# Kernel tuning notes

Hardware: AMD Instinct MI355X
Metric: run time of the kernel (lower is better)

Reference implementation:

```python
import jax, jax.numpy as jnp
import numpy as np

DIM = 1024
HEADS = 16
B, N = 4, 2048


def setup_inputs() -> dict:
    key = jax.random.key(0)
    ks = jax.random.split(key, 6)
    scale = DIM ** -0.5
    return {
        "x": jax.random.normal(ks[0], (B, N, DIM), dtype=jnp.float32),
        "mask": jax.random.randint(ks[1], (B, N, N), 0, 2) > 0,
        "Wqkv": jax.random.normal(ks[2], (DIM, 3 * DIM), dtype=jnp.float32) * scale,
        "bqkv": jax.random.normal(ks[3], (3 * DIM,), dtype=jnp.float32) * 0.02,
        "Wproj": jax.random.normal(ks[4], (DIM, DIM), dtype=jnp.float32) * scale,
        "bproj": jax.random.normal(ks[5], (DIM,), dtype=jnp.float32) * 0.02,
    }


def reference(x, mask, Wqkv, bqkv, Wproj, bproj):
    Bs, Ns, C = x.shape
    H = HEADS
    D = C // H
    scale = D ** -0.5
    qkv = x @ Wqkv + bqkv                       # [B, N, 3C]
    qkv = qkv.reshape(Bs, Ns, 3, H, D)          # split (three h d)
    q, k, v = jnp.moveaxis(qkv, 2, 0)           # each [B, N, H, D]
    q = q.transpose(0, 2, 1, 3)                 # [B, H, N, D]
    k = k.transpose(0, 2, 1, 3)
    v = v.transpose(0, 2, 1, 3)
    attn = jnp.einsum("bhnd,bhmd->bhnm", q, k) * scale  # [B, H, N, N]
    attn = jnp.where(mask[:, None, :, :], -jnp.inf, attn)
    attn = jax.nn.softmax(attn, axis=-1)
    out = jnp.einsum("bhnm,bhmd->bhnd", attn, v)        # [B, H, N, D]
    out = out.transpose(0, 2, 1, 3).reshape(Bs, Ns, C)  # [B, N, C]
    return out @ Wproj + bproj
```

## Files before the change

### kernel.cpp

```cpp
#include <hip/hip_runtime.h>
#include <cstdint>
#include <cstddef>

constexpr int kC = 1024;
constexpr int kH = 16;
constexpr int kB = 4;
constexpr int kN = 2048;
constexpr int kD = 64;

typedef unsigned short u16;
typedef unsigned int   u32;
typedef unsigned long long u64;
typedef __bf16 v8bf  __attribute__((ext_vector_type(8)));
typedef float  v4f   __attribute__((ext_vector_type(4)));
typedef u16    u16x8 __attribute__((ext_vector_type(8)));
typedef u16    u16x4 __attribute__((ext_vector_type(4)));

__device__ inline u16 f2bf(float f) {
    union { float f; unsigned u; } v; v.f = f;
    unsigned r = v.u + 0x7FFFu + ((v.u >> 16) & 1u);
    return (u16)(r >> 16);
}

__device__ inline void gl2lds16(const u16* g, u16* l) {
    __builtin_amdgcn_global_load_lds(
        (const __attribute__((address_space(1))) void*)g,
        (__attribute__((address_space(3))) void*)l, 16, 0, 0);
}

__global__ __launch_bounds__(256) void cast_bf16_kernel(
    const float* __restrict__ in, u16* __restrict__ outp)
{
    const int i = blockIdx.x * 256 + threadIdx.x;
    const float4 f = ((const float4*)in)[i];
    u16x4 o;
    o.x = f2bf(f.x); o.y = f2bf(f.y); o.z = f2bf(f.z); o.w = f2bf(f.w);
    ((u16x4*)outp)[i] = o;
}

__global__ __launch_bounds__(256) void tpose_cast_kernel(
    const float* __restrict__ W, u16* __restrict__ Wt, int R, int Cc)
{
    __shared__ u16 tile[64][65];
    const int c0 = blockIdx.x * 64;
    const int r0 = blockIdx.y * 64;
    const int t  = threadIdx.x;
#pragma unroll
    for (int it = 0; it < 16; ++it) {
        const int r = it * 4 + (t >> 6);
        const int c = t & 63;
        tile[c][r] = f2bf(W[(size_t)(r0 + r) * Cc + c0 + c]);
    }
    __syncthreads();
#pragma unroll
    for (int it = 0; it < 16; ++it) {
        const int rr = it * 4 + (t >> 6);
        const int cc = t & 63;
        Wt[(size_t)(c0 + rr) * R + r0 + cc] = tile[rr][cc];
    }
}

__global__ __launch_bounds__(256) void maskpack_kernel(
    const int* __restrict__ mask, u32* __restrict__ bits)
{
    const int seg  = blockIdx.x * 4 + (threadIdx.x >> 6);
    const int lane = threadIdx.x & 63;
    const size_t row = (size_t)(seg >> 5);
    const int s = seg & 31;
    const int m = mask[row * kN + s * 64 + lane];
    const u64 bal = __ballot(m != 0);
    if (lane == 0) ((u64*)bits)[row * 32 + s] = bal;
}

template <int MODE>
__global__ __launch_bounds__(256) void gemm_mfma_kernel(
    const u16* __restrict__ A, const u16* __restrict__ Bt,
    const float* __restrict__ bias, float* __restrict__ Cout,
    u16* __restrict__ qOut, u16* __restrict__ kOut, u16* __restrict__ vOut,
    int M, int N, int K)
{
    __shared__ u16 As[128 * 32];
    __shared__ u16 Bs[128 * 32];
    const int t    = threadIdx.x;
    const int w    = t >> 6;
    const int lane = t & 63;
    const int quad = lane >> 4;
    const int l16  = lane & 15;
    const int m0   = blockIdx.y * 128;
    const int n0   = blockIdx.x * 128;

    const int sr = lane >> 2;
    const int sk = (lane & 3) * 8;
    const u16* Ag0 = A  + (size_t)(m0 + 32 * w      + sr) * K + sk;
    const u16* Ag1 = A  + (size_t)(m0 + 32 * w + 16 + sr) * K + sk;
    const u16* Bg0 = Bt + (size_t)(n0 + 32 * w      + sr) * K + sk;
    const u16* Bg1 = Bt + (size_t)(n0 + 32 * w + 16 + sr) * K + sk;
    u16* Al0 = &As[(32 * w)      * 32];
    u16* Al1 = &As[(32 * w + 16) * 32];
    u16* Bl0 = &Bs[(32 * w)      * 32];
    u16* Bl1 = &Bs[(32 * w + 16) * 32];

    v4f acc[4][4];
#pragma unroll
    for (int r = 0; r < 4; ++r)
#pragma unroll
        for (int c = 0; c < 4; ++c) acc[r][c] = (v4f){0.f, 0.f, 0.f, 0.f};

    const int mrow = (w >> 1) * 64;
    const int ncol = (w & 1) * 64;

    for (int k0 = 0; k0 < K; k0 += 32) {
        __syncthreads();
        gl2lds16(Ag0 + k0, Al0);
        gl2lds16(Ag1 + k0, Al1);
        gl2lds16(Bg0 + k0, Bl0);
        gl2lds16(Bg1 + k0, Bl1);
        __syncthreads();

        v8bf af[4], bfr[4];
#pragma unroll
        for (int r = 0; r < 4; ++r)
            af[r] = *(const v8bf*)(&As[(mrow + r * 16 + l16) * 32 + quad * 8]);
#pragma unroll
        for (int c = 0; c < 4; ++c)
            bfr[c] = *(const v8bf*)(&Bs[(ncol + c * 16 + l16) * 32 + quad * 8]);
#pragma unroll
        for (int r = 0; r < 4; ++r)
#pragma unroll
            for (int c = 0; c < 4; ++c)
                acc[r][c] = __builtin_amdgcn_mfma_f32_16x16x32_bf16(
                    af[r], bfr[c], acc[r][c], 0, 0, 0);
    }

#pragma unroll
    for (int r = 0; r < 4; ++r) {
#pragma unroll
        for (int c = 0; c < 4; ++c) {
            const int col = n0 + ncol + c * 16 + l16;
            const float bv = bias[col];
#pragma unroll
            for (int reg = 0; reg < 4; ++reg) {
                const int row = m0 + mrow + r * 16 + quad * 4 + reg;
                const float val = acc[r][c][reg] + bv;
                if (MODE == 0) {
                    Cout[(size_t)row * N + col] = val;
                } else {
                    const int which = col >> 10;
                    const int rem   = col & 1023;
                    const int h     = rem >> 6;
                    const int d     = rem & 63;
                    const int b     = row >> 11;
                    const int n     = row & 2047;
                    u16* dst = (which == 0) ? qOut : (which == 1) ? kOut : vOut;
                    dst[(((size_t)(b * kH + h)) * kN + n) * kD + d] = f2bf(val);
                }
            }
        }
    }
}

__global__ __launch_bounds__(256, 3) void attn_mfma_kernel(
    const u16* __restrict__ q, const u16* __restrict__ k,
    const u16* __restrict__ v, const u32* __restrict__ mbits,
    u16* __restrict__ out)
{
    __shared__ u16 Ks[128 * 64];
    __shared__ u16 Vt[64 * 128];
    __shared__ u16 Ps[64 * 128];

    const int t    = threadIdx.x;
    const int w    = t >> 6;
    const int lane = t & 63;
    const int quad = lane >> 4;
    const int l16  = lane & 15;

    const int bh    = blockIdx.x >> 5;
    const int tile0 = (blockIdx.x & 31) * 64;
    const int b     = bh >> 4;
    const int h     = bh & 15;

    const u16* qb = q + (size_t)bh * kN * kD;
    const u16* kb = k + (size_t)bh * kN * kD;
    const u16* vb = v + (size_t)bh * kN * kD;

    const int qrow = tile0 + w * 16 + l16;
    const v8bf qf0 = *(const v8bf*)(qb + (size_t)qrow * kD + quad * 8);
    const v8bf qf1 = *(const v8bf*)(qb + (size_t)qrow * kD + 32 + quad * 8);

    const u32* mrowb = mbits + ((size_t)b * kN + qrow) * 64;

    const int skr  = t >> 1;
    const int skh  = t & 1;
    const int svk  = t >> 3;
    const int svd  = t & 7;
    const u16* kgp = kb + (size_t)skr * kD + skh * 32;
    const u16* vgp = vb + (size_t)(svk * 4) * kD + svd * 8;

    u16x8 kpre[4], vpre[4];
    uint4 mpre;
    auto prefetch = [&](int k0) {
        const u16x8* ks = (const u16x8*)(kgp + (size_t)k0 * kD);
        kpre[0] = ks[0]; kpre[1] = ks[1]; kpre[2] = ks[2]; kpre[3] = ks[3];
        const u16* vs = vgp + (size_t)k0 * kD;
        vpre[0] = *(const u16x8*)(vs);
        vpre[1] = *(const u16x8*)(vs + kD);
        vpre[2] = *(const u16x8*)(vs + 2 * kD);
        vpre[3] = *(const u16x8*)(vs + 3 * kD);
        mpre = *(const uint4*)(mrowb + (k0 >> 5));
    };

    v4f oacc[4];
#pragma unroll
    for (int i = 0; i < 4; ++i) oacc[i] = (v4f){0.f, 0.f, 0.f, 0.f};
    float rs = 0.f;

    prefetch(0);

    for (int kt = 0; kt < kN / 128; ++kt) {
        u16x8 kcur[4], vcur[4];
#pragma unroll
        for (int i = 0; i < 4; ++i) { kcur[i] = kpre[i]; vcur[i] = vpre[i]; }
        const uint4 mcur = mpre;
        const u32 mw[4] = {mcur.x, mcur.y, mcur.z, mcur.w};
        if (kt + 1 < kN / 128) prefetch((kt + 1) * 128);

        __syncthreads();

        {
            const int cb = skh * 4;
            u16* drow = &Ks[skr * 64];
#pragma unroll
            for (int i = 0; i < 4; ++i)
                *(u16x8*)(&drow[((cb + i) ^ (skr & 7)) * 8]) = kcur[i];
        }
        {
            const int blk = svk >> 1;
            const int off = (svk & 1) * 4;
#pragma unroll
            for (int j = 0; j < 8; ++j) {
                const int d = svd * 8 + j;
                u16x4 p;
                p.x = vcur[0][j]; p.y = vcur[1][j]; p.z = vcur[2][j]; p.w = vcur[3][j];
                *(u16x4*)(&Vt[d * 128 + ((blk ^ (d & 15)) * 8) + off]) = p;
            }
        }
        __syncthreads();

#pragma unroll
        for (int nb = 0; nb < 8; ++nb) {
            const int krow = nb * 16 + l16;
            const v8bf kf0 = *(const v8bf*)(&Ks[krow * 64 + ((quad       ^ (krow & 7)) * 8)]);
            const v8bf kf1 = *(const v8bf*)(&Ks[krow * 64 + (((quad + 4) ^ (krow & 7)) * 8)]);
            v4f s = (v4f){0.f, 0.f, 0.f, 0.f};
            s = __builtin_amdgcn_mfma_f32_16x16x32_bf16(kf0, qf0, s, 0, 0, 0);
            s = __builtin_amdgcn_mfma_f32_16x16x32_bf16(kf1, qf1, s, 0, 0, 0);

            const u32 m4 = (mw[nb >> 1] >> ((nb & 1) * 16 + quad * 4)) & 0xFu;
            const float e0 = (m4 & 1u) ? 0.f : __expf(s[0] * 0.125f);
            const float e1 = (m4 & 2u) ? 0.f : __expf(s[1] * 0.125f);
            const float e2 = (m4 & 4u) ? 0.f : __expf(s[2] * 0.125f);
            const float e3 = (m4 & 8u) ? 0.f : __expf(s[3] * 0.125f);
            rs += (e0 + e1) + (e2 + e3);

            u16x4 pw; pw.x = f2bf(e0); pw.y = f2bf(e1); pw.z = f2bf(e2); pw.w = f2bf(e3);
            const int pblk = nb * 2 + (quad >> 1);
            *(u16x4*)(&Ps[(w * 16 + l16) * 128 + ((pblk ^ l16) * 8) + (quad & 1) * 4]) = pw;
        }

#pragma unroll
        for (int ks = 0; ks < 4; ++ks) {
            const v8bf pa = *(const v8bf*)(&Ps[(w * 16 + l16) * 128 + (((ks * 4 + quad) ^ l16) * 8)]);
#pragma unroll
            for (int db = 0; db < 4; ++db) {
                const int d = db * 16 + l16;
                const v8bf vf = *(const v8bf*)(&Vt[d * 128 + (((ks * 4 + quad) ^ (d & 15)) * 8)]);
                oacc[db] = __builtin_amdgcn_mfma_f32_16x16x32_bf16(pa, vf, oacc[db], 0, 0, 0);
            }
        }
    }

    rs += __shfl_xor(rs, 16);
    rs += __shfl_xor(rs, 32);
    const float inv = 1.f / rs;
    float rq[4];
#pragma unroll
    for (int reg = 0; reg < 4; ++reg)
        rq[reg] = __shfl(inv, quad * 4 + reg);

#pragma unroll
    for (int db = 0; db < 4; ++db) {
#pragma unroll
        for (int reg = 0; reg < 4; ++reg) {
            const int row = tile0 + w * 16 + quad * 4 + reg;
            const int col = h * 64 + db * 16 + l16;
            out[((size_t)(b * kN + row)) * kC + col] = f2bf(oacc[db][reg] * rq[reg]);
        }
    }
}

extern "C" void kernel_launch(void* const* d_in, const int* in_sizes, int n_in,
                              void* d_out, int out_size, void* d_ws, size_t ws_size,
                              hipStream_t stream)
{
    const float* x     = (const float*)d_in[0];
    const int*   mask  = (const int*)d_in[1];
    const float* Wqkv  = (const float*)d_in[2];
    const float* bqkv  = (const float*)d_in[3];
    const float* Wproj = (const float*)d_in[4];
    const float* bproj = (const float*)d_in[5];
    float* out = (float*)d_out;

    const size_t nx = (size_t)kB * kN * kC;
    const size_t qkv_elems = (size_t)kB * kH * kN * kD;
    u16* xb     = (u16*)d_ws;
    u16* qbuf   = xb + nx;
    u16* kbuf   = qbuf + qkv_elems;
    u16* vbuf   = kbuf + qkv_elems;
    u16* aob    = vbuf + qkv_elems;
    u16* Wqkvt  = aob + nx;
    u16* Wprojt = Wqkvt + (size_t)3 * kC * kC;
    u32* mbits  = (u32*)(Wprojt + (size_t)kC * kC);

    maskpack_kernel<<<dim3(kB * kN * 32 / 4), dim3(256), 0, stream>>>(mask, mbits);
    cast_bf16_kernel<<<dim3(nx / 1024), dim3(256), 0, stream>>>(x, xb);
    tpose_cast_kernel<<<dim3(3 * kC / 64, kC / 64), dim3(256), 0, stream>>>(
        Wqkv, Wqkvt, kC, 3 * kC);
    tpose_cast_kernel<<<dim3(kC / 64, kC / 64), dim3(256), 0, stream>>>(
        Wproj, Wprojt, kC, kC);

    gemm_mfma_kernel<1><<<dim3(3 * kC / 128, kB * kN / 128), dim3(256), 0, stream>>>(
        xb, Wqkvt, bqkv, nullptr, qbuf, kbuf, vbuf, kB * kN, 3 * kC, kC);

    attn_mfma_kernel<<<dim3(kB * kH * (kN / 64)), dim3(256), 0, stream>>>(
        qbuf, kbuf, vbuf, mbits, aob);

    gemm_mfma_kernel<0><<<dim3(kC / 128, kB * kN / 128), dim3(256), 0, stream>>>(
        aob, Wprojt, bproj, out, nullptr, nullptr, nullptr, kB * kN, kC, kC);
}
```

Before: 443.1 us.

## Halve attention KV tile to 64, raise occupancy, use exp2 and packed bf16 conversion

```diff
diff --git a/kernel.cpp b/kernel.cpp
--- a/kernel.cpp
+++ b/kernel.cpp
@@ -15,12 +15,28 @@
 typedef float  v4f   __attribute__((ext_vector_type(4)));
 typedef u16    u16x8 __attribute__((ext_vector_type(8)));
 typedef u16    u16x4 __attribute__((ext_vector_type(4)));
-
-__device__ inline u16 f2bf(float f) {
-    union { float f; unsigned u; } v; v.f = f;
-    unsigned r = v.u + 0x7FFFu + ((v.u >> 16) & 1u);
-    return (u16)(r >> 16);
-}
+typedef u16    u16x2 __attribute__((ext_vector_type(2)));
+
+__device__ inline u32 f2bf_pk(float a, float b) {
+#if __has_builtin(__builtin_amdgcn_cvt_pk_bf16_f32)
+    return __builtin_bit_cast(u32, __builtin_amdgcn_cvt_pk_bf16_f32(a, b));
+#else
+    union { float f; u32 u; } x, y; x.f = a; y.f = b;
+    const u32 ra = (x.u + 0x7FFFu + ((x.u >> 16) & 1u)) >> 16;
+    const u32 rb = (y.u + 0x7FFFu + ((y.u >> 16) & 1u)) >> 16;
+    return ra | (rb << 16);
+#endif
+}
+__device__ inline u16 f2bf(float f) { return (u16)(f2bf_pk(f, f) & 0xffffu); }
+
+__device__ inline float fexp2(float x) {
+#if __has_builtin(__builtin_amdgcn_exp2f)
+    return __builtin_amdgcn_exp2f(x);
+#else
+    return exp2f(x);
+#endif
+}
+constexpr float kScaleLog2e = 0.18033688011112042f;
 
 __device__ inline void gl2lds16(const u16* g, u16* l) {
     __builtin_amdgcn_global_load_lds(
@@ -33,9 +49,8 @@
 {
     const int i = blockIdx.x * 256 + threadIdx.x;
     const float4 f = ((const float4*)in)[i];
-    u16x4 o;
-    o.x = f2bf(f.x); o.y = f2bf(f.y); o.z = f2bf(f.z); o.w = f2bf(f.w);
-    ((u16x4*)outp)[i] = o;
+    uint2 o; o.x = f2bf_pk(f.x, f.y); o.y = f2bf_pk(f.z, f.w);
+    ((uint2*)outp)[i] = o;
 }
 
 __global__ __launch_bounds__(256) void tpose_cast_kernel(
@@ -159,14 +174,14 @@
     }
 }
 
-__global__ __launch_bounds__(256, 3) void attn_mfma_kernel(
+__global__ __launch_bounds__(256, 6) void attn_mfma_kernel(
     const u16* __restrict__ q, const u16* __restrict__ k,
     const u16* __restrict__ v, const u32* __restrict__ mbits,
     u16* __restrict__ out)
 {
-    __shared__ u16 Ks[128 * 64];
-    __shared__ u16 Vt[64 * 128];
-    __shared__ u16 Ps[64 * 128];
+    __shared__ u16 Ks[64 * 64];
+    __shared__ u16 Vt[64 * 64];
+    __shared__ u16 Ps[64 * 64];
 
     const int t    = threadIdx.x;
     const int w    = t >> 6;
@@ -189,24 +204,27 @@
 
     const u32* mrowb = mbits + ((size_t)b * kN + qrow) * 64;
 
-    const int skr  = t >> 1;
-    const int skh  = t & 1;
-    const int svk  = t >> 3;
-    const int svd  = t & 7;
-    const u16* kgp = kb + (size_t)skr * kD + skh * 32;
-    const u16* vgp = vb + (size_t)(svk * 4) * kD + svd * 8;
-
-    u16x8 kpre[4], vpre[4];
-    uint4 mpre;
+    const int skr = t & 63;
+    const int skb = (t >> 6) * 2;
+    const u16* kgp = kb + (size_t)skr * kD + skb * 8;
+    const int svk = (t & 31) * 2;
+    const int svd = (t >> 5) * 8;
+    const u16* vgp = vb + (size_t)svk * kD + svd;
+
+    u16* kdst0 = &Ks[skr * 64 + (((skb)     ^ (skr & 7)) * 8)];
+    u16* kdst1 = &Ks[skr * 64 + (((skb + 1) ^ (skr & 7)) * 8)];
+
+    u16x8 kpre0, kpre1, vpre0, vpre1;
+    u32 mp0, mp1;
     auto prefetch = [&](int k0) {
-        const u16x8* ks = (const u16x8*)(kgp + (size_t)k0 * kD);
-        kpre[0] = ks[0]; kpre[1] = ks[1]; kpre[2] = ks[2]; kpre[3] = ks[3];
-        const u16* vs = vgp + (size_t)k0 * kD;
-        vpre[0] = *(const u16x8*)(vs);
-        vpre[1] = *(const u16x8*)(vs + kD);
-        vpre[2] = *(const u16x8*)(vs + 2 * kD);
-        vpre[3] = *(const u16x8*)(vs + 3 * kD);
-        mpre = *(const uint4*)(mrowb + (k0 >> 5));
+        const u16* kp = kgp + (size_t)k0 * kD;
+        kpre0 = *(const u16x8*)(kp);
+        kpre1 = *(const u16x8*)(kp + 8);
+        const u16* vp = vgp + (size_t)k0 * kD;
+        vpre0 = *(const u16x8*)(vp);
+        vpre1 = *(const u16x8*)(vp + kD);
+        const uint2 mm = *(const uint2*)(mrowb + (k0 >> 5));
+        mp0 = mm.x; mp1 = mm.y;
     };
 
     v4f oacc[4];
@@ -216,64 +234,52 @@
 
     prefetch(0);
 
-    for (int kt = 0; kt < kN / 128; ++kt) {
-        u16x8 kcur[4], vcur[4];
-#pragma unroll
-        for (int i = 0; i < 4; ++i) { kcur[i] = kpre[i]; vcur[i] = vpre[i]; }
-        const uint4 mcur = mpre;
-        const u32 mw[4] = {mcur.x, mcur.y, mcur.z, mcur.w};
-        if (kt + 1 < kN / 128) prefetch((kt + 1) * 128);
-
+    for (int kt = 0; kt < kN / 64; ++kt) {
         __syncthreads();
 
-        {
-            const int cb = skh * 4;
-            u16* drow = &Ks[skr * 64];
-#pragma unroll
-            for (int i = 0; i < 4; ++i)
-                *(u16x8*)(&drow[((cb + i) ^ (skr & 7)) * 8]) = kcur[i];
-        }
-        {
-            const int blk = svk >> 1;
-            const int off = (svk & 1) * 4;
-#pragma unroll
-            for (int j = 0; j < 8; ++j) {
-                const int d = svd * 8 + j;
-                u16x4 p;
-                p.x = vcur[0][j]; p.y = vcur[1][j]; p.z = vcur[2][j]; p.w = vcur[3][j];
-                *(u16x4*)(&Vt[d * 128 + ((blk ^ (d & 15)) * 8) + off]) = p;
-            }
-        }
+        *(u16x8*)kdst0 = kpre0;
+        *(u16x8*)kdst1 = kpre1;
+#pragma unroll
+        for (int j = 0; j < 8; ++j) {
+            u16x2 p; p.x = vpre0[j]; p.y = vpre1[j];
+            *(u16x2*)(&Vt[(svd + j) * 64 + (((svk >> 3) ^ j) * 8) + (svk & 7)]) = p;
+        }
+        const u32 mc0 = mp0, mc1 = mp1;
         __syncthreads();
 
-#pragma unroll
-        for (int nb = 0; nb < 8; ++nb) {
+        if (kt + 1 < kN / 64) prefetch((kt + 1) * 64);
+
+#pragma unroll
+        for (int nb = 0; nb < 4; ++nb) {
             const int krow = nb * 16 + l16;
-            const v8bf kf0 = *(const v8bf*)(&Ks[krow * 64 + ((quad       ^ (krow & 7)) * 8)]);
+            const v8bf kf0 = *(const v8bf*)(&Ks[krow * 64 + (((quad)     ^ (krow & 7)) * 8)]);
             const v8bf kf1 = *(const v8bf*)(&Ks[krow * 64 + (((quad + 4) ^ (krow & 7)) * 8)]);
             v4f s = (v4f){0.f, 0.f, 0.f, 0.f};
             s = __builtin_amdgcn_mfma_f32_16x16x32_bf16(kf0, qf0, s, 0, 0, 0);
             s = __builtin_amdgcn_mfma_f32_16x16x32_bf16(kf1, qf1, s, 0, 0, 0);
 
-            const u32 m4 = (mw[nb >> 1] >> ((nb & 1) * 16 + quad * 4)) & 0xFu;
-            const float e0 = (m4 & 1u) ? 0.f : __expf(s[0] * 0.125f);
-            const float e1 = (m4 & 2u) ? 0.f : __expf(s[1] * 0.125f);
-            const float e2 = (m4 & 4u) ? 0.f : __expf(s[2] * 0.125f);
-            const float e3 = (m4 & 8u) ? 0.f : __expf(s[3] * 0.125f);
+            const u32 m4 = ((nb < 2 ? mc0 : mc1) >> ((nb & 1) * 16 + quad * 4)) & 0xFu;
+            const float e0 = (m4 & 1u) ? 0.f : fexp2(s[0] * kScaleLog2e);
+            const float e1 = (m4 & 2u) ? 0.f : fexp2(s[1] * kScaleLog2e);
+            const float e2 = (m4 & 4u) ? 0.f : fexp2(s[2] * kScaleLog2e);
+            const float e3 = (m4 & 8u) ? 0.f : fexp2(s[3] * kScaleLog2e);
             rs += (e0 + e1) + (e2 + e3);
 
-            u16x4 pw; pw.x = f2bf(e0); pw.y = f2bf(e1); pw.z = f2bf(e2); pw.w = f2bf(e3);
-            const int pblk = nb * 2 + (quad >> 1);
-            *(u16x4*)(&Ps[(w * 16 + l16) * 128 + ((pblk ^ l16) * 8) + (quad & 1) * 4]) = pw;
-        }
-
-#pragma unroll
-        for (int ks = 0; ks < 4; ++ks) {
-            const v8bf pa = *(const v8bf*)(&Ps[(w * 16 + l16) * 128 + (((ks * 4 + quad) ^ l16) * 8)]);
+            union { u32 wds[2]; u16x4 v4; } pk;
+            pk.wds[0] = f2bf_pk(e0, e1);
+            pk.wds[1] = f2bf_pk(e2, e3);
+            *(u16x4*)(&Ps[(w * 16 + l16) * 64 +
+                          (((nb * 2 + (quad >> 1)) ^ (l16 & 7)) * 8) + (quad & 1) * 4]) = pk.v4;
+        }
+
+#pragma unroll
+        for (int ks = 0; ks < 2; ++ks) {
+            const v8bf pa = *(const v8bf*)(&Ps[(w * 16 + l16) * 64 +
+                                               (((ks * 4 + quad) ^ (l16 & 7)) * 8)]);
 #pragma unroll
             for (int db = 0; db < 4; ++db) {
                 const int d = db * 16 + l16;
-                const v8bf vf = *(const v8bf*)(&Vt[d * 128 + (((ks * 4 + quad) ^ (d & 15)) * 8)]);
+                const v8bf vf = *(const v8bf*)(&Vt[d * 64 + (((ks * 4 + quad) ^ (d & 7)) * 8)]);
                 oacc[db] = __builtin_amdgcn_mfma_f32_16x16x32_bf16(pa, vf, oacc[db], 0, 0, 0);
             }
         }
```

New measurement: 453.9 us. 2.4% more time.
